# Performance work log

Measured on AMD Instinct MI355X. Metric: run time of the kernel, lower is better.

Reference implementation:

```python
import jax, jax.numpy as jnp
import numpy as np

# TFMBSLinear forward: quantize input and weight to ternary {-1,0,1} via sign,
# compute out = sign(x) @ sign(W)^T (what the ternary fabric T-GEMV kernel
# computes, with zero-skip), then add float bias. The base-3 byte packing is a
# transport encoding only; the math is the ternary matmul.

def setup_inputs() -> dict:
    key = jax.random.key(0)
    k1, k2, k3 = jax.random.split(key, 3)
    B, IN, OUT = 8192, 2048, 2048
    x = jax.random.normal(k1, (B, IN), dtype=jnp.float32)
    # kaiming-uniform-ish init; only sign matters for the fabric kernel
    weight = jax.random.normal(k2, (OUT, IN), dtype=jnp.float32)
    fan_in_bound = 1.0 / np.sqrt(IN)
    bias = jax.random.uniform(k3, (OUT,), dtype=jnp.float32,
                              minval=-fan_in_bound, maxval=fan_in_bound)
    return {"input": x, "weight": weight, "bias": bias}

def reference(input, weight, bias):
    x_t = jnp.sign(input)    # ternary activations [B, IN]
    w_t = jnp.sign(weight)   # ternary weights     [OUT, IN]
    out = jnp.einsum('bi,oi->bo', x_t, w_t)  # T-GEMV accumulation, fp32
    return out + bias
```

## Files before the change

kernel.cpp:

```cpp
#include <hip/hip_runtime.h>
#include <hip/hip_bf16.h>


typedef int intx4 __attribute__((ext_vector_type(4)));

static constexpr int M = 8192;
static constexpr int N = 2048;
static constexpr int K = 2048;
static constexpr int BM = 128, BN = 128, BK = 64;

__device__ __forceinline__ unsigned sgn_b(float v) {
    return (unsigned)(unsigned char)((v > 0.0f) ? 1 : ((v < 0.0f) ? -1 : 0));
}

__global__ __launch_bounds__(256) void quant_sign_i8(
    const float4* __restrict__ x, const float4* __restrict__ w,
    char* __restrict__ qx, char* __restrict__ qw, int nx8, int ntot8)
{
    int i = blockIdx.x * 256 + threadIdx.x;
    if (i >= ntot8) return;
    const float4* src;
    char* dst;
    if (i < nx8) { src = x + (size_t)i * 2; dst = qx + (size_t)i * 8; }
    else {
        int j = i - nx8;
        src = w + (size_t)j * 2; dst = qw + (size_t)j * 8;
    }
    float4 a = src[0], b = src[1];
    uint2 p;
    p.x = sgn_b(a.x) | (sgn_b(a.y) << 8) | (sgn_b(a.z) << 16) | (sgn_b(a.w) << 24);
    p.y = sgn_b(b.x) | (sgn_b(b.y) << 8) | (sgn_b(b.z) << 16) | (sgn_b(b.w) << 24);
    *reinterpret_cast<uint2*>(dst) = p;
}

__global__ __launch_bounds__(256, 3) void tgemm_i8(
    const char* __restrict__ A,
    const char* __restrict__ B,
    const float* __restrict__ bias,
    float* __restrict__ C)
{
    __shared__ char sA[BM * BK];
    __shared__ char sB[BN * BK];

    const int tid  = threadIdx.x;
    const int wave = tid >> 6;
    const int lane = tid & 63;
    const int quad = lane >> 4;
    const int l16  = lane & 15;

    const int bm = blockIdx.x * BM;
    const int bn = blockIdx.y * BN;

    const int c0 = tid;
    const int c1 = tid + 256;
    const int r0 = c0 >> 2, kc0 = (c0 & 3) ^ (r0 & 3);
    const int r1 = c1 >> 2, kc1 = (c1 & 3) ^ (r1 & 3);
    const char* gA0 = A + (size_t)(bm + r0) * K + kc0 * 16;
    const char* gA1 = A + (size_t)(bm + r1) * K + kc1 * 16;
    const char* gB0 = B + (size_t)(bn + r0) * K + kc0 * 16;
    const char* gB1 = B + (size_t)(bn + r1) * K + kc1 * 16;

    char* lA0 = sA + wave * 1024;
    char* lA1 = sA + 4096 + wave * 1024;
    char* lB0 = sB + wave * 1024;
    char* lB1 = sB + 4096 + wave * 1024;

    const int wm = (wave & 1) * 64;
    const int wn = (wave >> 1) * 64;

    const int aoff = (wm + l16) * BK + ((quad ^ (l16 & 3)) * 16);
    const int boff = (wn + l16) * BK + ((quad ^ (l16 & 3)) * 16);

    intx4 acc[4][4] = {};

    for (int k0 = 0; k0 < K; k0 += BK) {
        __builtin_amdgcn_global_load_lds(
            (const __attribute__((address_space(1))) void*)(gA0 + k0),
            (__attribute__((address_space(3))) void*)lA0, 16, 0, 0);
        __builtin_amdgcn_global_load_lds(
            (const __attribute__((address_space(1))) void*)(gA1 + k0),
            (__attribute__((address_space(3))) void*)lA1, 16, 0, 0);
        __builtin_amdgcn_global_load_lds(
            (const __attribute__((address_space(1))) void*)(gB0 + k0),
            (__attribute__((address_space(3))) void*)lB0, 16, 0, 0);
        __builtin_amdgcn_global_load_lds(
            (const __attribute__((address_space(1))) void*)(gB1 + k0),
            (__attribute__((address_space(3))) void*)lB1, 16, 0, 0);

        __syncthreads();

        intx4 af[4], bfr[4];
        #pragma unroll
        for (int i = 0; i < 4; ++i)
            af[i] = *reinterpret_cast<const intx4*>(&sA[aoff + i * 16 * BK]);
        #pragma unroll
        for (int j = 0; j < 4; ++j)
            bfr[j] = *reinterpret_cast<const intx4*>(&sB[boff + j * 16 * BK]);

        #pragma unroll
        for (int i = 0; i < 4; ++i) {
            #pragma unroll
            for (int j = 0; j < 4; ++j) {
                acc[i][j] = __builtin_amdgcn_mfma_i32_16x16x64_i8(
                    af[i], bfr[j], acc[i][j], 0, 0, 0);
            }
        }
        __syncthreads();
    }

    const int cn = bn + wn + l16;
    float bcol[4];
    #pragma unroll
    for (int j = 0; j < 4; ++j) bcol[j] = bias[cn + j * 16];

    const int cm = bm + wm + quad * 4;
    #pragma unroll
    for (int i = 0; i < 4; ++i) {
        #pragma unroll
        for (int j = 0; j < 4; ++j) {
            #pragma unroll
            for (int r = 0; r < 4; ++r) {
                C[(size_t)(cm + i * 16 + r) * N + (cn + j * 16)] =
                    (float)acc[i][j][r] + bcol[j];
            }
        }
    }
}

extern "C" void kernel_launch(void* const* d_in, const int* in_sizes, int n_in,
                              void* d_out, int out_size, void* d_ws, size_t ws_size,
                              hipStream_t stream) {
    const float* x    = (const float*)d_in[0];
    const float* w    = (const float*)d_in[1];
    const float* bias = (const float*)d_in[2];
    float* out = (float*)d_out;

    char* qx = (char*)d_ws;
    char* qw = qx + (size_t)M * K;

    const int nx8   = (M * K) / 8;
    const int ntot8 = nx8 + (N * K) / 8;
    quant_sign_i8<<<(ntot8 + 255) / 256, 256, 0, stream>>>(
        (const float4*)x, (const float4*)w, qx, qw, nx8, ntot8);

    dim3 grid(M / BM, N / BN);
    tgemm_i8<<<grid, 256, 0, stream>>>(qx, qw, bias, out);
}
```

Measured before the change: 163.2 us.

## Encode ternary values as FP4 and use scaled 32x32x64 FP4 MFMA

Ternary signs are packed as FP4 (E2M1) nibbles, with 1.0 encoded as 0x2 plus a sign bit, instead of int8 bytes. The GEMM now runs the MX-scaled f8f6f4 MFMA in FP4 mode at 32x32x64 with unit scales and fp32 accumulation. This halves the quantized operand footprint and global/LDS traffic, and moves to a denser matrix instruction. Each wave now computes a 2x2 grid of 32x32 tiles, and the LDS read pattern and epilogue mapping change to match. The main risk is an incorrect FP4 lane/K layout or swizzle producing wrong results; exactness itself holds because integer sums up to 2048 are exact in fp32.

Measured after the change: 146.0 us. -10.5%, faster.

```diff
diff --git a/kernel.cpp b/kernel.cpp
--- a/kernel.cpp
+++ b/kernel.cpp
@@ -2,51 +2,58 @@
 #include <hip/hip_bf16.h>
 
 
-typedef int intx4 __attribute__((ext_vector_type(4)));
+typedef int   intx4    __attribute__((ext_vector_type(4)));
+typedef int   intx8    __attribute__((ext_vector_type(8)));
+typedef float floatx16 __attribute__((ext_vector_type(16)));
 
 static constexpr int M = 8192;
 static constexpr int N = 2048;
 static constexpr int K = 2048;
-static constexpr int BM = 128, BN = 128, BK = 64;
+static constexpr int KB = K / 2;
+static constexpr int BM = 128, BN = 128;
+static constexpr int BKB = 64;
 
-__device__ __forceinline__ unsigned sgn_b(float v) {
-    return (unsigned)(unsigned char)((v > 0.0f) ? 1 : ((v < 0.0f) ? -1 : 0));
+__device__ __forceinline__ unsigned nib(float v) {
+    unsigned u = __float_as_uint(v);
+    return (v != 0.0f) ? (0x2u | ((u >> 28) & 0x8u)) : 0u;
 }
 
-__global__ __launch_bounds__(256) void quant_sign_i8(
+__global__ __launch_bounds__(256) void quant_sign_fp4(
     const float4* __restrict__ x, const float4* __restrict__ w,
-    char* __restrict__ qx, char* __restrict__ qw, int nx8, int ntot8)
+    uint2* __restrict__ qx, uint2* __restrict__ qw, int nx16, int ntot16)
 {
     int i = blockIdx.x * 256 + threadIdx.x;
-    if (i >= ntot8) return;
+    if (i >= ntot16) return;
     const float4* src;
-    char* dst;
-    if (i < nx8) { src = x + (size_t)i * 2; dst = qx + (size_t)i * 8; }
-    else {
-        int j = i - nx8;
-        src = w + (size_t)j * 2; dst = qw + (size_t)j * 8;
-    }
-    float4 a = src[0], b = src[1];
-    uint2 p;
-    p.x = sgn_b(a.x) | (sgn_b(a.y) << 8) | (sgn_b(a.z) << 16) | (sgn_b(a.w) << 24);
-    p.y = sgn_b(b.x) | (sgn_b(b.y) << 8) | (sgn_b(b.z) << 16) | (sgn_b(b.w) << 24);
-    *reinterpret_cast<uint2*>(dst) = p;
+    uint2* dst;
+    if (i < nx16) { src = x + (size_t)i * 4; dst = qx + i; }
+    else { int j = i - nx16; src = w + (size_t)j * 4; dst = qw + j; }
+    float4 v0 = src[0], v1 = src[1], v2 = src[2], v3 = src[3];
+    unsigned lo = nib(v0.x)        | (nib(v0.y) << 4)  | (nib(v0.z) << 8)  | (nib(v0.w) << 12)
+                | (nib(v1.x) << 16)| (nib(v1.y) << 20) | (nib(v1.z) << 24) | (nib(v1.w) << 28);
+    unsigned hi = nib(v2.x)        | (nib(v2.y) << 4)  | (nib(v2.z) << 8)  | (nib(v2.w) << 12)
+                | (nib(v3.x) << 16)| (nib(v3.y) << 20) | (nib(v3.z) << 24) | (nib(v3.w) << 28);
+    *dst = make_uint2(lo, hi);
 }
 
-__global__ __launch_bounds__(256, 3) void tgemm_i8(
+__device__ __forceinline__ intx8 ext4(intx4 v) {
+    return __builtin_shufflevector(v, v, 0, 1, 2, 3, -1, -1, -1, -1);
+}
+
+__global__ __launch_bounds__(256, 3) void tgemm_fp4(
     const char* __restrict__ A,
     const char* __restrict__ B,
     const float* __restrict__ bias,
     float* __restrict__ C)
 {
-    __shared__ char sA[BM * BK];
-    __shared__ char sB[BN * BK];
+    __shared__ char sA[BM * BKB];
+    __shared__ char sB[BN * BKB];
 
     const int tid  = threadIdx.x;
     const int wave = tid >> 6;
     const int lane = tid & 63;
-    const int quad = lane >> 4;
-    const int l16  = lane & 15;
+    const int l32  = lane & 31;
+    const int half = lane >> 5;
 
     const int bm = blockIdx.x * BM;
     const int bn = blockIdx.y * BN;
@@ -55,10 +62,10 @@
     const int c1 = tid + 256;
     const int r0 = c0 >> 2, kc0 = (c0 & 3) ^ (r0 & 3);
     const int r1 = c1 >> 2, kc1 = (c1 & 3) ^ (r1 & 3);
-    const char* gA0 = A + (size_t)(bm + r0) * K + kc0 * 16;
-    const char* gA1 = A + (size_t)(bm + r1) * K + kc1 * 16;
-    const char* gB0 = B + (size_t)(bn + r0) * K + kc0 * 16;
-    const char* gB1 = B + (size_t)(bn + r1) * K + kc1 * 16;
+    const char* gA0 = A + (size_t)(bm + r0) * KB + kc0 * 16;
+    const char* gA1 = A + (size_t)(bm + r1) * KB + kc1 * 16;
+    const char* gB0 = B + (size_t)(bn + r0) * KB + kc0 * 16;
+    const char* gB1 = B + (size_t)(bn + r1) * KB + kc1 * 16;
 
     char* lA0 = sA + wave * 1024;
     char* lA1 = sA + 4096 + wave * 1024;
@@ -68,61 +75,71 @@
     const int wm = (wave & 1) * 64;
     const int wn = (wave >> 1) * 64;
 
-    const int aoff = (wm + l16) * BK + ((quad ^ (l16 & 3)) * 16);
-    const int boff = (wn + l16) * BK + ((quad ^ (l16 & 3)) * 16);
+    const int sw    = l32 & 3;
+    const int slot0 = (0 + half) ^ sw;
+    const int slot1 = (2 + half) ^ sw;
+    const int arow  = (wm + l32) * BKB;
+    const int brow  = (wn + l32) * BKB;
 
-    intx4 acc[4][4] = {};
+    floatx16 acc[2][2] = {};
 
-    for (int k0 = 0; k0 < K; k0 += BK) {
+    for (int kb = 0; kb < KB; kb += BKB) {
         __builtin_amdgcn_global_load_lds(
-            (const __attribute__((address_space(1))) void*)(gA0 + k0),
+            (const __attribute__((address_space(1))) void*)(gA0 + kb),
             (__attribute__((address_space(3))) void*)lA0, 16, 0, 0);
         __builtin_amdgcn_global_load_lds(
-            (const __attribute__((address_space(1))) void*)(gA1 + k0),
+            (const __attribute__((address_space(1))) void*)(gA1 + kb),
             (__attribute__((address_space(3))) void*)lA1, 16, 0, 0);
         __builtin_amdgcn_global_load_lds(
-            (const __attribute__((address_space(1))) void*)(gB0 + k0),
+            (const __attribute__((address_space(1))) void*)(gB0 + kb),
             (__attribute__((address_space(3))) void*)lB0, 16, 0, 0);
         __builtin_amdgcn_global_load_lds(
-            (const __attribute__((address_space(1))) void*)(gB1 + k0),
+            (const __attribute__((address_space(1))) void*)(gB1 + kb),
             (__attribute__((address_space(3))) void*)lB1, 16, 0, 0);
 
         __syncthreads();
 
-        intx4 af[4], bfr[4];
-        #pragma unroll
-        for (int i = 0; i < 4; ++i)
-            af[i] = *reinterpret_cast<const intx4*>(&sA[aoff + i * 16 * BK]);
-        #pragma unroll
-        for (int j = 0; j < 4; ++j)
-            bfr[j] = *reinterpret_cast<const intx4*>(&sB[boff + j * 16 * BK]);
+        intx4 a0t0 = *reinterpret_cast<const intx4*>(&sA[arow        + slot0 * 16]);
+        intx4 a1t0 = *reinterpret_cast<const intx4*>(&sA[arow + 2048 + slot0 * 16]);
+        intx4 b0t0 = *reinterpret_cast<const intx4*>(&sB[brow        + slot0 * 16]);
+        intx4 b1t0 = *reinterpret_cast<const intx4*>(&sB[brow + 2048 + slot0 * 16]);
+        intx4 a0t1 = *reinterpret_cast<const intx4*>(&sA[arow        + slot1 * 16]);
+        intx4 a1t1 = *reinterpret_cast<const intx4*>(&sA[arow + 2048 + slot1 * 16]);
+        intx4 b0t1 = *reinterpret_cast<const intx4*>(&sB[brow        + slot1 * 16]);
+        intx4 b1t1 = *reinterpret_cast<const intx4*>(&sB[brow + 2048 + slot1 * 16]);
 
-        #pragma unroll
-        for (int i = 0; i < 4; ++i) {
-            #pragma unroll
-            for (int j = 0; j < 4; ++j) {
-                acc[i][j] = __builtin_amdgcn_mfma_i32_16x16x64_i8(
-                    af[i], bfr[j], acc[i][j], 0, 0, 0);
-            }
-        }
+        acc[0][0] = __builtin_amdgcn_mfma_scale_f32_32x32x64_f8f6f4(
+            ext4(a0t0), ext4(b0t0), acc[0][0], 4, 4, 0, 127, 0, 127);
+        acc[0][1] = __builtin_amdgcn_mfma_scale_f32_32x32x64_f8f6f4(
+            ext4(a0t0), ext4(b1t0), acc[0][1], 4, 4, 0, 127, 0, 127);
+        acc[1][0] = __builtin_amdgcn_mfma_scale_f32_32x32x64_f8f6f4(
+            ext4(a1t0), ext4(b0t0), acc[1][0], 4, 4, 0, 127, 0, 127);
+        acc[1][1] = __builtin_amdgcn_mfma_scale_f32_32x32x64_f8f6f4(
+            ext4(a1t0), ext4(b1t0), acc[1][1], 4, 4, 0, 127, 0, 127);
+        acc[0][0] = __builtin_amdgcn_mfma_scale_f32_32x32x64_f8f6f4(
+            ext4(a0t1), ext4(b0t1), acc[0][0], 4, 4, 0, 127, 0, 127);
+        acc[0][1] = __builtin_amdgcn_mfma_scale_f32_32x32x64_f8f6f4(
+            ext4(a0t1), ext4(b1t1), acc[0][1], 4, 4, 0, 127, 0, 127);
+        acc[1][0] = __builtin_amdgcn_mfma_scale_f32_32x32x64_f8f6f4(
+            ext4(a1t1), ext4(b0t1), acc[1][0], 4, 4, 0, 127, 0, 127);
+        acc[1][1] = __builtin_amdgcn_mfma_scale_f32_32x32x64_f8f6f4(
+            ext4(a1t1), ext4(b1t1), acc[1][1], 4, 4, 0, 127, 0, 127);
+
         __syncthreads();
     }
 
-    const int cn = bn + wn + l16;
-    float bcol[4];
+    const int cn0 = bn + wn + l32;
+    const float bc0 = bias[cn0];
+    const float bc1 = bias[cn0 + 32];
+    const int rbase = bm + wm + 4 * half;
+
     #pragma unroll
-    for (int j = 0; j < 4; ++j) bcol[j] = bias[cn + j * 16];
-
-    const int cm = bm + wm + quad * 4;
-    #pragma unroll
-    for (int i = 0; i < 4; ++i) {
+    for (int i = 0; i < 2; ++i) {
         #pragma unroll
-        for (int j = 0; j < 4; ++j) {
-            #pragma unroll
-            for (int r = 0; r < 4; ++r) {
-                C[(size_t)(cm + i * 16 + r) * N + (cn + j * 16)] =
-                    (float)acc[i][j][r] + bcol[j];
-            }
+        for (int r = 0; r < 16; ++r) {
+            const int row = rbase + 32 * i + (r & 3) + 8 * (r >> 2);
+            C[(size_t)row * N + cn0]      = acc[i][0][r] + bc0;
+            C[(size_t)row * N + cn0 + 32] = acc[i][1][r] + bc1;
         }
     }
 }
@@ -136,13 +153,13 @@
     float* out = (float*)d_out;
 
     char* qx = (char*)d_ws;
-    char* qw = qx + (size_t)M * K;
+    char* qw = qx + (size_t)M * KB;
 
-    const int nx8   = (M * K) / 8;
-    const int ntot8 = nx8 + (N * K) / 8;
-    quant_sign_i8<<<(ntot8 + 255) / 256, 256, 0, stream>>>(
-        (const float4*)x, (const float4*)w, qx, qw, nx8, ntot8);
+    const int nx16   = (M * K) / 16;
+    const int ntot16 = nx16 + (N * K) / 16;
+    quant_sign_fp4<<<ntot16 / 256, 256, 0, stream>>>(
+        (const float4*)x, (const float4*)w, (uint2*)qx, (uint2*)qw, nx16, ntot16);
 
     dim3 grid(M / BM, N / BN);
-    tgemm_i8<<<grid, 256, 0, stream>>>(qx, qw, bias, out);
+    tgemm_fp4<<<grid, 256, 0, stream>>>(qx, qw, bias, out);
 }
```
